# Kernel optimization log

Hardware: AMD Instinct MI355X
Metric: run time of the kernel (lower is better)

## Reference

```python
import jax, jax.numpy as jnp
import numpy as np
import math

B = 8192
D_MODEL = 1
D_STATE = 16
D_CONV = 4
EXPAND = 2
NSLICES = 4
NFEAT = 256
NTRIP = 100
D_INNER = EXPAND * D_MODEL
DT_RANK = math.ceil(D_MODEL / 16)
EPS = 1e-5


def setup_inputs():
    key = jax.random.key(0)
    ks = iter(jax.random.split(key, 64))
    def rn(shape, s=0.1):
        return jax.random.normal(next(ks), shape, dtype=jnp.float32) * s
    dt_bias0 = jnp.float32(math.log(math.expm1(0.01)))  # standard mamba dt init
    A_init = jnp.log(jnp.tile(jnp.arange(1, D_STATE + 1, dtype=jnp.float32), (D_INNER, 1)))
    inp = {}
    inp['x'] = jax.random.normal(next(ks), (B, NFEAT), dtype=jnp.float32)
    inp['norm_w'] = jnp.ones((D_MODEL,), jnp.float32)
    inp['norm_b'] = rn((D_MODEL,), 0.1)
    inp['in_proj_w'] = rn((2 * D_INNER, D_MODEL), 0.5)
    for d in ('f', 'b', 's'):
        inp['conv_w_' + d] = rn((D_INNER, D_CONV), 0.5)
        inp['conv_b_' + d] = rn((D_INNER,), 0.1)
        inp['xproj_w_' + d] = rn((DT_RANK + 2 * D_STATE, D_INNER), 0.3)
        inp['dtproj_w_' + d] = rn((D_INNER, DT_RANK), 0.3)
        inp['dtproj_b_' + d] = rn((D_INNER,), 0.05) + dt_bias0
        inp['A_log_' + d] = A_init + rn((D_INNER, D_STATE), 0.01)
        inp['Dskip_' + d] = jnp.ones((D_INNER,), jnp.float32) + rn((D_INNER,), 0.01)
    inp['out_proj_w'] = rn((D_MODEL, D_INNER), 0.3)
    inp['w1'] = rn((512, NFEAT), 0.05); inp['b1'] = rn((512,), 0.05)
    inp['w2'] = rn((256, 512), 0.05); inp['b2'] = rn((256,), 0.05)
    inp['w3'] = rn((NTRIP, 256), 0.05); inp['b3'] = rn((NTRIP,), 0.05)
    return inp


def _mamba_dir(xz, conv_w, conv_b, xproj_w, dtproj_w, dtproj_b, A_log, Dskip):
    # xz: [b, 2*d_inner, l] -> y: [b, d_inner, l]; one causal selective scan.
    b, _, l = xz.shape
    x, z = jnp.split(xz, 2, axis=1)
    x = jax.lax.conv_general_dilated(
        x, conv_w[:, None, :], (1,), [(D_CONV - 1, 0)],
        dimension_numbers=('NCH', 'OIH', 'NCH'), feature_group_count=D_INNER)
    x = jax.nn.silu(x + conv_b[None, :, None])               # [b, d, l]
    xdbl = jnp.einsum('bdl,kd->bkl', x, xproj_w)             # [b, r+2n, l]
    delta = jax.nn.softplus(
        jnp.einsum('brl,dr->bdl', xdbl[:, :DT_RANK], dtproj_w) + dtproj_b[None, :, None])
    Bs = xdbl[:, DT_RANK:DT_RANK + D_STATE]                  # [b, n, l]
    Cs = xdbl[:, DT_RANK + D_STATE:]                         # [b, n, l]
    A = -jnp.exp(A_log)                                      # [d, n]

    def step(h, inp):
        dlt, u, Bt, Ct = inp                                 # [b,d],[b,d],[b,n],[b,n]
        h = jnp.exp(dlt[..., None] * A) * h + (dlt * u)[..., None] * Bt[:, None, :]
        return h, jnp.einsum('bdn,bn->bd', h, Ct)

    h0 = jnp.zeros((b, D_INNER, D_STATE), x.dtype)
    _, ys = jax.lax.scan(step, h0, (delta.transpose(2, 0, 1), x.transpose(2, 0, 1),
                                    Bs.transpose(2, 0, 1), Cs.transpose(2, 0, 1)))
    y = ys.transpose(1, 2, 0) + x * Dskip[None, :, None]
    return y * jax.nn.silu(z)


def reference(x, norm_w, norm_b, in_proj_w,
              conv_w_f, conv_b_f, xproj_w_f, dtproj_w_f, dtproj_b_f, A_log_f, Dskip_f,
              conv_w_b, conv_b_b, xproj_w_b, dtproj_w_b, dtproj_b_b, A_log_b, Dskip_b,
              conv_w_s, conv_b_s, xproj_w_s, dtproj_w_s, dtproj_b_s, A_log_s, Dskip_s,
              out_proj_w, w1, b1, w2, b2, w3, b3):
    h = x[:, :, None]                                        # [B, L, 1]
    mu = h.mean(-1, keepdims=True)
    var = ((h - mu) ** 2).mean(-1, keepdims=True)
    hn = (h - mu) / jnp.sqrt(var + EPS) * norm_w + norm_b    # LayerNorm over dim=1
    xz = jnp.einsum('bld,ed->bel', hn, in_proj_w)            # [B, 2*d_inner, L]
    b, c, l = xz.shape
    out_f = _mamba_dir(xz, conv_w_f, conv_b_f, xproj_w_f, dtproj_w_f, dtproj_b_f, A_log_f, Dskip_f)
    out_b = jnp.flip(_mamba_dir(jnp.flip(xz, -1), conv_w_b, conv_b_b, xproj_w_b,
                                dtproj_w_b, dtproj_b_b, A_log_b, Dskip_b), -1)
    # slice interleave: chunk(nslices, -1) -> stack(-1) -> flatten(-2)
    xz_s = xz.reshape(b, c, NSLICES, l // NSLICES).transpose(0, 1, 3, 2).reshape(b, c, l)
    out_s = _mamba_dir(xz_s, conv_w_s, conv_b_s, xproj_w_s, dtproj_w_s, dtproj_b_s, A_log_s, Dskip_s)
    out_s = out_s.reshape(b, D_INNER, NSLICES, l // NSLICES).transpose(0, 1, 3, 2).reshape(b, D_INNER, l)
    y = jnp.einsum('bdl,ed->ble', out_f + out_b + out_s, out_proj_w)  # [B, L, 1]
    y = y[:, :, 0]                                           # transpose(-1,-2).squeeze(1)
    h1 = jax.nn.elu(y @ w1.T + b1)
    h2 = jax.nn.elu(h1 @ w2.T + b2)
    return h2 @ w3.T + b3
```

## Files before the change

### kernel.cpp

```cpp
#include <hip/hip_runtime.h>
#include <math.h>

#define SEQL 256

struct P1 {
    const float* norm_b;
    const float* in_proj_w;
    const float* conv_w[3];
    const float* conv_b[3];
    const float* xproj_w[3];
    const float* dtproj_w[3];
    const float* dtproj_b[3];
    const float* A_log[3];
    const float* Dskip[3];
    const float* out_proj_w;
    float* yrow;
};

__device__ __forceinline__ float silu_f(float x)     { return x / (1.0f + expf(-x)); }
__device__ __forceinline__ float softplus_f(float x) { return x > 0.f ? x + log1pf(expf(-x)) : log1pf(expf(x)); }
__device__ __forceinline__ float elu_f(float x)      { return x > 0.f ? x : expm1f(x); }

__global__ __launch_bounds__(256) void k_row(P1 p) {
    __shared__ float xs[3][2][SEQL];
    __shared__ float dl[3][2][SEQL];
    __shared__ float hc[SEQL][49];

    const int tid = threadIdx.x;
    const float nb0 = p.norm_b[0];
    const float c0  = nb0 * p.in_proj_w[0];
    const float c1  = nb0 * p.in_proj_w[1];

    {
        const int l = tid;
        for (int dir = 0; dir < 3; ++dir) {
            const float* cw  = p.conv_w[dir];
            const float* cb  = p.conv_b[dir];
            const float* xp  = p.xproj_w[dir];
            const float* dtw = p.dtproj_w[dir];
            const float* dtb = p.dtproj_b[dir];
            float xsv[2];
            for (int d = 0; d < 2; ++d) {
                float s = 0.f;
                for (int k = 0; k < 4; ++k)
                    if (l - 3 + k >= 0) s += cw[d * 4 + k];
                const float xc = (d == 0 ? c0 : c1) * s + cb[d];
                xsv[d] = silu_f(xc);
                xs[dir][d][l] = xsv[d];
            }
            const float xd0 = xp[0] * xsv[0] + xp[1] * xsv[1];
            dl[dir][0][l] = softplus_f(dtw[0] * xd0 + dtb[0]);
            dl[dir][1][l] = softplus_f(dtw[1] * xd0 + dtb[1]);
        }
    }
    __syncthreads();

    if (tid < 48) {
        const int dir = tid / 16;
        const int r   = tid % 16;
        const int d   = r / 8;
        const int k   = r % 8;
        const int n0  = 2 * k, n1 = 2 * k + 1;
        const float* xp = p.xproj_w[dir];
        const float A0 = -expf(p.A_log[dir][d * 16 + n0]);
        const float A1 = -expf(p.A_log[dir][d * 16 + n1]);
        const float b00 = xp[(1 + n0) * 2],      b01 = xp[(1 + n0) * 2 + 1];
        const float b10 = xp[(1 + n1) * 2],      b11 = xp[(1 + n1) * 2 + 1];
        const float c00 = xp[(17 + n0) * 2],     c01 = xp[(17 + n0) * 2 + 1];
        const float c10 = xp[(17 + n1) * 2],     c11 = xp[(17 + n1) * 2 + 1];
        const int q = (dir * 2 + d) * 8 + k;
        float h0 = 0.f, h1 = 0.f;
        for (int l = 0; l < SEQL; ++l) {
            const float x0 = xs[dir][0][l], x1 = xs[dir][1][l];
            const float dlt = dl[dir][d][l];
            const float u   = (d == 0) ? x0 : x1;
            const float du  = dlt * u;
            h0 = expf(dlt * A0) * h0 + du * (b00 * x0 + b01 * x1);
            h1 = expf(dlt * A1) * h1 + du * (b10 * x0 + b11 * x1);
            hc[l][q] = h0 * (c00 * x0 + c01 * x1) + h1 * (c10 * x0 + c11 * x1);
        }
    }
    __syncthreads();

    {
        const int t = tid;
        const float opw0 = p.out_proj_w[0], opw1 = p.out_proj_w[1];
        const float sz0  = silu_f(nb0 * p.in_proj_w[2]);
        const float sz1  = silu_f(nb0 * p.in_proj_w[3]);
        float acc = 0.f;
        for (int dir = 0; dir < 3; ++dir) {
            int lv;
            if      (dir == 0) lv = t;
            else if (dir == 1) lv = SEQL - 1 - t;
            else               lv = ((t & 3) << 6) + (t >> 2);
            float s0 = 0.f, s1 = 0.f;
            for (int k = 0; k < 8; ++k) {
                s0 += hc[lv][dir * 16 + k];
                s1 += hc[lv][dir * 16 + 8 + k];
            }
            const float y0 = (s0 + xs[dir][0][lv] * p.Dskip[dir][0]) * sz0;
            const float y1 = (s1 + xs[dir][1][lv] * p.Dskip[dir][1]) * sz1;
            acc += opw0 * y0 + opw1 * y1;
        }
        p.yrow[t] = acc;
    }
}

__global__ __launch_bounds__(64) void k_mlp1(const float* __restrict__ w1, const float* __restrict__ b1,
                                             const float* __restrict__ yrow, float* __restrict__ h1) {
    const int j = blockIdx.x, t = threadIdx.x;
    const float4 w = reinterpret_cast<const float4*>(w1)[j * 64 + t];
    const float4 y = reinterpret_cast<const float4*>(yrow)[t];
    float s = w.x * y.x + w.y * y.y + w.z * y.z + w.w * y.w;
    for (int m = 1; m < 64; m <<= 1) s += __shfl_xor(s, m);
    if (t == 0) h1[j] = elu_f(s + b1[j]);
}

__global__ __launch_bounds__(64) void k_mlp2(const float* __restrict__ w2, const float* __restrict__ b2,
                                             const float* __restrict__ h1, float* __restrict__ h2) {
    const int j = blockIdx.x, t = threadIdx.x;
    const float4* wr = reinterpret_cast<const float4*>(w2 + j * 512);
    const float4* hv = reinterpret_cast<const float4*>(h1);
    const float4 a = wr[t],      x = hv[t];
    const float4 b = wr[t + 64], y = hv[t + 64];
    float s = a.x * x.x + a.y * x.y + a.z * x.z + a.w * x.w
            + b.x * y.x + b.y * y.y + b.z * y.z + b.w * y.w;
    for (int m = 1; m < 64; m <<= 1) s += __shfl_xor(s, m);
    if (t == 0) h2[j] = elu_f(s + b2[j]);
}

__global__ __launch_bounds__(64) void k_mlp3(const float* __restrict__ w3, const float* __restrict__ b3,
                                             const float* __restrict__ h2, float* __restrict__ row) {
    const int j = blockIdx.x, t = threadIdx.x;
    const float4 w = reinterpret_cast<const float4*>(w3 + j * 256)[t];
    const float4 h = reinterpret_cast<const float4*>(h2)[t];
    float s = w.x * h.x + w.y * h.y + w.z * h.z + w.w * h.w;
    for (int m = 1; m < 64; m <<= 1) s += __shfl_xor(s, m);
    if (t == 0) row[j] = s + b3[j];
}

__global__ __launch_bounds__(256) void k_bcast(const float4* __restrict__ row4,
                                               float4* __restrict__ out4, int total4) {
    const int idx = blockIdx.x * blockDim.x + threadIdx.x;
    if (idx < total4) out4[idx] = row4[idx % 25];
}

extern "C" void kernel_launch(void* const* d_in, const int* in_sizes, int n_in,
                              void* d_out, int out_size, void* d_ws, size_t ws_size,
                              hipStream_t stream) {
    const float* const* in = (const float* const*)d_in;
    P1 p;
    p.norm_b    = in[2];
    p.in_proj_w = in[3];
    for (int dir = 0; dir < 3; ++dir) {
        const int base = 4 + dir * 7;
        p.conv_w[dir]   = in[base + 0];
        p.conv_b[dir]   = in[base + 1];
        p.xproj_w[dir]  = in[base + 2];
        p.dtproj_w[dir] = in[base + 3];
        p.dtproj_b[dir] = in[base + 4];
        p.A_log[dir]    = in[base + 5];
        p.Dskip[dir]    = in[base + 6];
    }
    p.out_proj_w = in[25];
    const float* w1 = in[26]; const float* b1 = in[27];
    const float* w2 = in[28]; const float* b2 = in[29];
    const float* w3 = in[30]; const float* b3 = in[31];

    float* ws   = (float*)d_ws;
    float* yrow = ws;
    float* h1   = ws + 256;
    float* h2   = ws + 768;
    float* row  = ws + 1024;
    p.yrow = yrow;

    k_row <<<1,   256, 0, stream>>>(p);
    k_mlp1<<<512, 64,  0, stream>>>(w1, b1, yrow, h1);
    k_mlp2<<<256, 64,  0, stream>>>(w2, b2, h1, h2);
    k_mlp3<<<100, 64,  0, stream>>>(w3, b3, h2, row);

    const int total4 = (8192 * 100) / 4;
    k_bcast<<<(total4 + 255) / 256, 256, 0, stream>>>(
        (const float4*)row, (float4*)d_out, total4);
}
```

Before: 156.1 us.

## Fuse scan row and three MLP layers into one single-block kernel

Merges the row-computation kernel and the three MLP layer kernels into one 1024-thread single-block kernel. Intermediates (yrow, h1, h2) stay in shared memory instead of a global workspace, and each MLP layer splits its dot products across threads with a partial-sum reduction. This removes three kernel launches and their global round trips. The cost is that about 1 MB of MLP weights is now streamed by a single compute unit instead of hundreds of blocks, which may be bandwidth-limited.

```diff
diff --git a/kernel.cpp b/kernel.cpp
--- a/kernel.cpp
+++ b/kernel.cpp
@@ -14,24 +14,33 @@
     const float* A_log[3];
     const float* Dskip[3];
     const float* out_proj_w;
-    float* yrow;
+    const float* w1; const float* b1;
+    const float* w2; const float* b2;
+    const float* w3; const float* b3;
+    float* row;
 };
 
 __device__ __forceinline__ float silu_f(float x)     { return x / (1.0f + expf(-x)); }
 __device__ __forceinline__ float softplus_f(float x) { return x > 0.f ? x + log1pf(expf(-x)) : log1pf(expf(x)); }
 __device__ __forceinline__ float elu_f(float x)      { return x > 0.f ? x : expm1f(x); }
 
-__global__ __launch_bounds__(256) void k_row(P1 p) {
-    __shared__ float xs[3][2][SEQL];
-    __shared__ float dl[3][2][SEQL];
-    __shared__ float hc[SEQL][49];
+__global__ __launch_bounds__(1024) void k_all(P1 p) {
+    __shared__ float S[15872];
+    float* xs   = S;
+    float* dl   = S + 1536;
+    float* hc   = S + 3072;
+    float* yrow = S + 15616;
+    float* part = S;
+    float* h1s  = S + 1024;
+    float* h2s  = S + 1536;
+    float* p3   = S + 1792;
 
     const int tid = threadIdx.x;
     const float nb0 = p.norm_b[0];
     const float c0  = nb0 * p.in_proj_w[0];
     const float c1  = nb0 * p.in_proj_w[1];
 
-    {
+    if (tid < SEQL) {
         const int l = tid;
         for (int dir = 0; dir < 3; ++dir) {
             const float* cw  = p.conv_w[dir];
@@ -46,11 +55,11 @@
                     if (l - 3 + k >= 0) s += cw[d * 4 + k];
                 const float xc = (d == 0 ? c0 : c1) * s + cb[d];
                 xsv[d] = silu_f(xc);
-                xs[dir][d][l] = xsv[d];
+                xs[(dir * 2 + d) * SEQL + l] = xsv[d];
             }
             const float xd0 = xp[0] * xsv[0] + xp[1] * xsv[1];
-            dl[dir][0][l] = softplus_f(dtw[0] * xd0 + dtb[0]);
-            dl[dir][1][l] = softplus_f(dtw[1] * xd0 + dtb[1]);
+            dl[(dir * 2 + 0) * SEQL + l] = softplus_f(dtw[0] * xd0 + dtb[0]);
+            dl[(dir * 2 + 1) * SEQL + l] = softplus_f(dtw[1] * xd0 + dtb[1]);
         }
     }
     __syncthreads();
@@ -64,25 +73,28 @@
         const float* xp = p.xproj_w[dir];
         const float A0 = -expf(p.A_log[dir][d * 16 + n0]);
         const float A1 = -expf(p.A_log[dir][d * 16 + n1]);
-        const float b00 = xp[(1 + n0) * 2],      b01 = xp[(1 + n0) * 2 + 1];
-        const float b10 = xp[(1 + n1) * 2],      b11 = xp[(1 + n1) * 2 + 1];
-        const float c00 = xp[(17 + n0) * 2],     c01 = xp[(17 + n0) * 2 + 1];
-        const float c10 = xp[(17 + n1) * 2],     c11 = xp[(17 + n1) * 2 + 1];
+        const float b00 = xp[(1 + n0) * 2],  b01 = xp[(1 + n0) * 2 + 1];
+        const float b10 = xp[(1 + n1) * 2],  b11 = xp[(1 + n1) * 2 + 1];
+        const float c00 = xp[(17 + n0) * 2], c01 = xp[(17 + n0) * 2 + 1];
+        const float c10 = xp[(17 + n1) * 2], c11 = xp[(17 + n1) * 2 + 1];
         const int q = (dir * 2 + d) * 8 + k;
+        const float* xs0 = xs + (dir * 2 + 0) * SEQL;
+        const float* xs1 = xs + (dir * 2 + 1) * SEQL;
+        const float* dld = dl + (dir * 2 + d) * SEQL;
         float h0 = 0.f, h1 = 0.f;
         for (int l = 0; l < SEQL; ++l) {
-            const float x0 = xs[dir][0][l], x1 = xs[dir][1][l];
-            const float dlt = dl[dir][d][l];
+            const float x0 = xs0[l], x1 = xs1[l];
+            const float dlt = dld[l];
             const float u   = (d == 0) ? x0 : x1;
             const float du  = dlt * u;
             h0 = expf(dlt * A0) * h0 + du * (b00 * x0 + b01 * x1);
             h1 = expf(dlt * A1) * h1 + du * (b10 * x0 + b11 * x1);
-            hc[l][q] = h0 * (c00 * x0 + c01 * x1) + h1 * (c10 * x0 + c11 * x1);
-        }
-    }
-    __syncthreads();
-
-    {
+            hc[l * 49 + q] = h0 * (c00 * x0 + c01 * x1) + h1 * (c10 * x0 + c11 * x1);
+        }
+    }
+    __syncthreads();
+
+    if (tid < SEQL) {
         const int t = tid;
         const float opw0 = p.out_proj_w[0], opw1 = p.out_proj_w[1];
         const float sz0  = silu_f(nb0 * p.in_proj_w[2]);
@@ -95,48 +107,66 @@
             else               lv = ((t & 3) << 6) + (t >> 2);
             float s0 = 0.f, s1 = 0.f;
             for (int k = 0; k < 8; ++k) {
-                s0 += hc[lv][dir * 16 + k];
-                s1 += hc[lv][dir * 16 + 8 + k];
+                s0 += hc[lv * 49 + dir * 16 + k];
+                s1 += hc[lv * 49 + dir * 16 + 8 + k];
             }
-            const float y0 = (s0 + xs[dir][0][lv] * p.Dskip[dir][0]) * sz0;
-            const float y1 = (s1 + xs[dir][1][lv] * p.Dskip[dir][1]) * sz1;
+            const float y0 = (s0 + xs[(dir * 2 + 0) * SEQL + lv] * p.Dskip[dir][0]) * sz0;
+            const float y1 = (s1 + xs[(dir * 2 + 1) * SEQL + lv] * p.Dskip[dir][1]) * sz1;
             acc += opw0 * y0 + opw1 * y1;
         }
-        p.yrow[t] = acc;
-    }
-}
-
-__global__ __launch_bounds__(64) void k_mlp1(const float* __restrict__ w1, const float* __restrict__ b1,
-                                             const float* __restrict__ yrow, float* __restrict__ h1) {
-    const int j = blockIdx.x, t = threadIdx.x;
-    const float4 w = reinterpret_cast<const float4*>(w1)[j * 64 + t];
-    const float4 y = reinterpret_cast<const float4*>(yrow)[t];
-    float s = w.x * y.x + w.y * y.y + w.z * y.z + w.w * y.w;
-    for (int m = 1; m < 64; m <<= 1) s += __shfl_xor(s, m);
-    if (t == 0) h1[j] = elu_f(s + b1[j]);
-}
-
-__global__ __launch_bounds__(64) void k_mlp2(const float* __restrict__ w2, const float* __restrict__ b2,
-                                             const float* __restrict__ h1, float* __restrict__ h2) {
-    const int j = blockIdx.x, t = threadIdx.x;
-    const float4* wr = reinterpret_cast<const float4*>(w2 + j * 512);
-    const float4* hv = reinterpret_cast<const float4*>(h1);
-    const float4 a = wr[t],      x = hv[t];
-    const float4 b = wr[t + 64], y = hv[t + 64];
-    float s = a.x * x.x + a.y * x.y + a.z * x.z + a.w * x.w
-            + b.x * y.x + b.y * y.y + b.z * y.z + b.w * y.w;
-    for (int m = 1; m < 64; m <<= 1) s += __shfl_xor(s, m);
-    if (t == 0) h2[j] = elu_f(s + b2[j]);
-}
-
-__global__ __launch_bounds__(64) void k_mlp3(const float* __restrict__ w3, const float* __restrict__ b3,
-                                             const float* __restrict__ h2, float* __restrict__ row) {
-    const int j = blockIdx.x, t = threadIdx.x;
-    const float4 w = reinterpret_cast<const float4*>(w3 + j * 256)[t];
-    const float4 h = reinterpret_cast<const float4*>(h2)[t];
-    float s = w.x * h.x + w.y * h.y + w.z * h.z + w.w * h.w;
-    for (int m = 1; m < 64; m <<= 1) s += __shfl_xor(s, m);
-    if (t == 0) row[j] = s + b3[j];
+        yrow[t] = acc;
+    }
+    __syncthreads();
+
+    {
+        const int j = tid >> 1, half = tid & 1;
+        const float4* wr = reinterpret_cast<const float4*>(p.w1 + j * 256 + half * 128);
+        const float4* yv = reinterpret_cast<const float4*>(yrow + half * 128);
+        float s = 0.f;
+        for (int k = 0; k < 32; ++k) {
+            const float4 w = wr[k], y = yv[k];
+            s += w.x * y.x + w.y * y.y + w.z * y.z + w.w * y.w;
+        }
+        part[tid] = s;
+    }
+    __syncthreads();
+    if (tid < 512) h1s[tid] = elu_f(part[2 * tid] + part[2 * tid + 1] + p.b1[tid]);
+    __syncthreads();
+
+    {
+        const int j = tid >> 2, q = tid & 3;
+        const float4* wr = reinterpret_cast<const float4*>(p.w2 + j * 512 + q * 128);
+        const float4* hv = reinterpret_cast<const float4*>(h1s + q * 128);
+        float s = 0.f;
+        for (int k = 0; k < 32; ++k) {
+            const float4 w = wr[k], h = hv[k];
+            s += w.x * h.x + w.y * h.y + w.z * h.z + w.w * h.w;
+        }
+        part[tid] = s;
+    }
+    __syncthreads();
+    if (tid < 256)
+        h2s[tid] = elu_f(part[4 * tid] + part[4 * tid + 1] + part[4 * tid + 2] +
+                         part[4 * tid + 3] + p.b2[tid]);
+    __syncthreads();
+
+    if (tid < 800) {
+        const int j = tid >> 3, oc = tid & 7;
+        const float4* wr = reinterpret_cast<const float4*>(p.w3 + j * 256 + oc * 32);
+        const float4* hv = reinterpret_cast<const float4*>(h2s + oc * 32);
+        float s = 0.f;
+        for (int k = 0; k < 8; ++k) {
+            const float4 w = wr[k], h = hv[k];
+            s += w.x * h.x + w.y * h.y + w.z * h.z + w.w * h.w;
+        }
+        p3[tid] = s;
+    }
+    __syncthreads();
+    if (tid < 100) {
+        float s = p.b3[tid];
+        for (int k = 0; k < 8; ++k) s += p3[tid * 8 + k];
+        p.row[tid] = s;
+    }
 }
 
 __global__ __launch_bounds__(256) void k_bcast(const float4* __restrict__ row4,
@@ -163,23 +193,14 @@
         p.Dskip[dir]    = in[base + 6];
     }
     p.out_proj_w = in[25];
-    const float* w1 = in[26]; const float* b1 = in[27];
-    const float* w2 = in[28]; const float* b2 = in[29];
-    const float* w3 = in[30]; const float* b3 = in[31];
-
-    float* ws   = (float*)d_ws;
-    float* yrow = ws;
-    float* h1   = ws + 256;
-    float* h2   = ws + 768;
-    float* row  = ws + 1024;
-    p.yrow = yrow;
-
-    k_row <<<1,   256, 0, stream>>>(p);
-    k_mlp1<<<512, 64,  0, stream>>>(w1, b1, yrow, h1);
-    k_mlp2<<<256, 64,  0, stream>>>(w2, b2, h1, h2);
-    k_mlp3<<<100, 64,  0, stream>>>(w3, b3, h2, row);
+    p.w1 = in[26]; p.b1 = in[27];
+    p.w2 = in[28]; p.b2 = in[29];
+    p.w3 = in[30]; p.b3 = in[31];
+    p.row = (float*)d_ws;
+
+    k_all<<<1, 1024, 0, stream>>>(p);
 
     const int total4 = (8192 * 100) / 4;
     k_bcast<<<(total4 + 255) / 256, 256, 0, stream>>>(
-        (const float4*)row, (float4*)d_out, total4);
+        (const float4*)d_ws, (float4*)d_out, total4);
 }
```

Measured after the change: 195.4 us. +25.2%, slower.
